# Performance work log

Hardware: AMD Instinct MI355X
Metric: run time of the kernel (lower is better)

Reference implementation:

```python
import jax, jax.numpy as jnp
import numpy as np

C = 64
N_H = 4
N_WIN = 16
WIN_L = 8   # compressor window length (overlapped)
WIN_S = 4   # compressor stride -> T//4 blocks


def _rms(x, eps=1e-6):
    return x * jax.lax.rsqrt(jnp.mean(x * x, axis=-1, keepdims=True) + eps)


def _rope(x, negate=False):
    # x: (..., L, D); rotate-half RoPE over positions 0..L-1
    L, D = x.shape[-2], x.shape[-1]
    half = D // 2
    inv_freq = 1.0 / (10000.0 ** (jnp.arange(half, dtype=x.dtype) / half))
    ang = jnp.arange(L, dtype=x.dtype)[:, None] * inv_freq  # (L, half)
    if negate:
        ang = -ang
    cos, sin = jnp.cos(ang), jnp.sin(ang)
    x1, x2 = x[..., :half], x[..., half:]
    return jnp.concatenate([x1 * cos - x2 * sin, x1 * sin + x2 * cos], axis=-1)


def _compress(H, W):
    # overlapped token compressor: windows of WIN_L, stride WIN_S, zero-pad tail
    B, T, d = H.shape
    Tc = T // WIN_S
    Hp = jnp.pad(H, ((0, 0), (0, WIN_L - WIN_S), (0, 0)))
    idx = WIN_S * jnp.arange(Tc)[:, None] + jnp.arange(WIN_L)[None, :]  # (Tc, WIN_L)
    win = Hp[:, idx]                       # (B, Tc, WIN_L, d)
    return win.reshape(B, Tc, WIN_L * d) @ W  # (B, Tc, out)


def setup_inputs() -> dict:
    key = jax.random.key(0)
    ks = jax.random.split(key, 11)
    B, T, d = 2, 2048, 256

    def w(k, shape, fan):
        return jax.random.normal(k, shape, jnp.float32) / np.float32(np.sqrt(fan))

    H = jax.random.normal(ks[0], (B, T, d), jnp.float32)
    return {
        'H': H,
        'Wc_comp': w(ks[1], (WIN_L * d, C), WIN_L * d),
        'Wc_idx': w(ks[2], (WIN_L * d, 32), WIN_L * d),
        'W_DQ': w(ks[3], (d, 64), d),
        'W_IUQ': w(ks[4], (64, 4 * 32), 64),
        'W_w': w(ks[5], (64, 4), 64),
        'W_Q': w(ks[6], (d, N_H * C), d),
        'W_KV': w(ks[7], (d, C), d),
        'g_q': jnp.ones((N_H, C), jnp.float32),
        'g_k': jnp.ones((C,), jnp.float32),
        'g_v': jnp.ones((C,), jnp.float32),
        'Wg0': w(ks[8], (2 * C, 64), 2 * C),
        'bg0': jnp.zeros((64,), jnp.float32),
        'Wg1': w(ks[9], (2 * C, 64), 2 * C),
        'bg1': jnp.zeros((64,), jnp.float32),
        'Wout': w(ks[10], (128, d), 128),
        'bout': jnp.zeros((d,), jnp.float32),
    }


def reference(H, Wc_comp, Wc_idx, W_DQ, W_IUQ, W_w, W_Q, W_KV,
              g_q, g_k, g_v, Wg0, bg0, Wg1, bg1, Wout, bout):
    B, T, d = H.shape
    Tc = T // 4
    k_top = min(8, Tc)

    # ---- lightning indexer ----
    H_dc = H @ W_DQ                                   # (B,T,64)
    Q_I = (H_dc @ W_IUQ).reshape(B, T, 4, 32)         # (B,T,4,32)
    W_Iw = (H_dc @ W_w)[..., None]                    # (B,T,4,1)
    K_I = _compress(H, Wc_idx)                        # (B,Tc,32)
    dot = jnp.einsum('bthc,bsc->bths', Q_I, K_I)      # (B,T,4,Tc)
    I_ts = (W_Iw * jax.nn.relu(dot)).sum(axis=2)      # (B,T,Tc)

    t = jnp.arange(T)[:, None]
    s = jnp.arange(Tc)[None, :]
    mask_I = jnp.where(4 * s <= t, 0.0, -jnp.inf)     # (T,Tc) causal over blocks
    _, topk_idx = jax.lax.top_k(I_ts + mask_I, k_top)  # (B,T,k)
    bI = jnp.arange(B)[:, None, None]
    tI = jnp.arange(T)[None, :, None]
    M_comp = jnp.full((B, T, Tc), -jnp.inf).at[bI, tI, topk_idx].set(0.0)

    # ---- compressed + sliding KV ----
    KV = jnp.concatenate([_compress(H, Wc_comp), H @ W_KV], axis=1)  # (B,Tc+T,C)

    Q = (H @ W_Q).reshape(B, T, N_H, C).transpose(0, 2, 1, 3)        # (B,nh,T,C)
    Q = _rms(Q) * g_q[None, :, None, :]
    K = _rms(KV) * g_k
    V = _rms(KV) * g_v
    Q = _rope(Q)
    K = _rope(K)
    V = _rope(V)

    S = jnp.einsum('bhtc,bsc->bhts', Q, K) / np.float32(np.sqrt(C))  # (B,nh,T,Tc+T)

    S_comp = S[..., :Tc] + M_comp[:, None]
    rel = t - jnp.arange(T)[None, :]
    mask_slide = jnp.where((rel >= 0) & (rel < N_WIN), 0.0, -jnp.inf)  # (T,T)
    S_slide = S[..., Tc:] + mask_slide

    P = jax.nn.softmax(jnp.concatenate([S_comp, S_slide], axis=-1), axis=-1)
    O = jnp.einsum('bhts,bsc->bhtc', P, V)            # (B,nh,T,C)
    O = _rope(O, negate=True)

    O0 = O[:, :2].transpose(0, 2, 1, 3).reshape(B, T, 2 * C)
    O1 = O[:, 2:].transpose(0, 2, 1, 3).reshape(B, T, 2 * C)
    p_all = jnp.concatenate([O0 @ Wg0 + bg0, O1 @ Wg1 + bg1], axis=-1)
    return p_all @ Wout + bout
```

## Files before the change

kernel.cpp:

```cpp
#include <hip/hip_runtime.h>
#include <hip/hip_bf16.h>
#include <math.h>

#define T_DIM 2048
#define B_DIM 2
#define D_DIM 256
#define TC 512
#define KV_LEN 2560

typedef __attribute__((ext_vector_type(8))) short bf16x8;
typedef __attribute__((ext_vector_type(4))) float f32x4;
typedef unsigned short ush;

__device__ __forceinline__ float wave_sum64(float v) {
#pragma unroll
    for (int off = 32; off > 0; off >>= 1) v += __shfl_xor(v, off, 64);
    return v;
}

__device__ __forceinline__ float rope_angle(int pos, int j) {
    float inv = powf(10000.0f, -(float)j * (1.0f / 32.0f));
    return (float)pos * inv;
}

__global__ __launch_bounds__(256) void k_prep(
    const float* __restrict__ H, const float* __restrict__ W_Q,
    const float* __restrict__ W_KV, const float* __restrict__ W_DQ,
    const float* __restrict__ Wc_comp, const float* __restrict__ Wc_idx,
    const float* __restrict__ Wg0, const float* __restrict__ bg0,
    const float* __restrict__ Wg1, const float* __restrict__ bg1,
    const float* __restrict__ Wout, const float* __restrict__ bout,
    ush* __restrict__ Ap, ush* __restrict__ Ac,
    ush* __restrict__ Bp, ush* __restrict__ Bc,
    ush* __restrict__ Bo, float* __restrict__ biascomb)
{
    int gid = blockIdx.x * 256 + threadIdx.x;
    float vals[8];
    ush* dst;
    bool lo_part;

    if (gid < 262144) {
        int tile = gid >> 10;
        int c = (gid >> 6) & 15;
        int l = gid & 63;
        int bt = tile * 16 + (l & 15);
        int kb = (c & 7) * 32 + (l >> 4) * 8;
        const float* src = H + (size_t)bt * 256 + kb;
#pragma unroll
        for (int j = 0; j < 8; ++j) vals[j] = src[j];
        lo_part = (c >= 8);
        dst = Ap + (size_t)gid * 8;
    } else if (gid < 786432) {
        int g = gid - 262144;
        int tile = g >> 13;
        int c = (g >> 6) & 127;
        int l = g & 63;
        int m = tile * 16 + (l & 15);
        int s = m & 511;
        int b = m >> 9;
        int k2b = (c & 63) * 32 + (l >> 4) * 8;
        int r4 = 4 * s + (k2b >> 8);
        int col = k2b & 255;
        if (r4 < T_DIM) {
            const float* src = H + ((size_t)b * T_DIM + r4) * 256 + col;
#pragma unroll
            for (int j = 0; j < 8; ++j) vals[j] = src[j];
        } else {
#pragma unroll
            for (int j = 0; j < 8; ++j) vals[j] = 0.f;
        }
        lo_part = (c >= 64);
        dst = Ac + (size_t)g * 8;
    } else if (gid < 811008) {
        int g = gid - 786432;
        int tile = g >> 10;
        int c = (g >> 6) & 15;
        int l = g & 63;
        int n = tile * 16 + (l & 15);
        int kb = (c & 7) * 32 + (l >> 4) * 8;
#pragma unroll
        for (int j = 0; j < 8; ++j) {
            int k = kb + j;
            float w;
            if (n < 256)      w = W_Q[(size_t)k * 256 + n];
            else if (n < 320) w = W_KV[(size_t)k * 64 + (n - 256)];
            else              w = W_DQ[(size_t)k * 64 + (n - 320)];
            vals[j] = w;
        }
        lo_part = (c >= 8);
        dst = Bp + (size_t)g * 8;
    } else if (gid < 860160) {
        int g = gid - 811008;
        int tile = g >> 13;
        int c = (g >> 6) & 127;
        int l = g & 63;
        int n = tile * 16 + (l & 15);
        int k2b = (c & 63) * 32 + (l >> 4) * 8;
#pragma unroll
        for (int j = 0; j < 8; ++j) {
            int k = k2b + j;
            vals[j] = (n < 64) ? Wc_comp[(size_t)k * 64 + n]
                               : Wc_idx[(size_t)k * 32 + (n - 64)];
        }
        lo_part = (c >= 64);
        dst = Bc + (size_t)g * 8;
    } else if (gid < 925696) {
        int g = gid - 860160;
        int k = g >> 8;
        int n = g & 255;
        float acc = 0.f;
        if (k < 128) {
            for (int i = 0; i < 64; ++i)
                acc = fmaf(Wg0[k * 64 + i], Wout[(size_t)i * 256 + n], acc);
        } else {
            for (int i = 0; i < 64; ++i)
                acc = fmaf(Wg1[(k - 128) * 64 + i], Wout[(size_t)(64 + i) * 256 + n], acc);
        }
        __hip_bfloat16 hb = __float2bfloat16(acc);
        float hif = __bfloat162float(hb);
        __hip_bfloat16 lb = __float2bfloat16(acc - hif);
        int tile = n >> 4;
        int chi = k >> 5;
        int lane2 = (n & 15) + 16 * ((k >> 3) & 3);
        int j = k & 7;
        Bo[(size_t)(tile * 16 + chi) * 512 + lane2 * 8 + j] = *(ush*)&hb;
        Bo[(size_t)(tile * 16 + chi + 8) * 512 + lane2 * 8 + j] = *(ush*)&lb;
        return;
    } else if (gid < 925952) {
        int n = gid - 925696;
        float acc = bout[n];
        for (int i = 0; i < 64; ++i) {
            acc = fmaf(bg0[i], Wout[(size_t)i * 256 + n], acc);
            acc = fmaf(bg1[i], Wout[(size_t)(64 + i) * 256 + n], acc);
        }
        biascomb[n] = acc;
        return;
    } else {
        return;
    }

    bf16x8 out8;
#pragma unroll
    for (int j = 0; j < 8; ++j) {
        float x = vals[j];
        __hip_bfloat16 hb = __float2bfloat16(x);
        if (!lo_part) {
            out8[j] = *(short*)&hb;
        } else {
            float hif = __bfloat162float(hb);
            __hip_bfloat16 lb = __float2bfloat16(x - hif);
            out8[j] = *(short*)&lb;
        }
    }
    *(bf16x8*)dst = out8;
}

__global__ __launch_bounds__(64) void k_mfma(
    const ush* __restrict__ Ap, const ush* __restrict__ Ac,
    const ush* __restrict__ Bp, const ush* __restrict__ Bc,
    float* __restrict__ Pre, float* __restrict__ Prec_part)
{
    int lane = threadIdx.x;
    int mrow = lane & 15;
    int q = lane >> 4;

    f32x4 acc[2][6];
#pragma unroll
    for (int mt = 0; mt < 2; ++mt)
#pragma unroll
        for (int nt = 0; nt < 6; ++nt) acc[mt][nt] = (f32x4){0.f, 0.f, 0.f, 0.f};

    if (blockIdx.x < 512) {
        int p = blockIdx.x;
        int m0 = (p >> 2) * 32;
        int n0 = (p & 3) * 96;
        int at0 = (m0 >> 4) * 16;
        int bt0n = (n0 >> 4) * 16;

        for (int c = 0; c < 8; ++c) {
            bf16x8 ahi[2], alo[2], bhi[6], blo[6];
#pragma unroll
            for (int mt = 0; mt < 2; ++mt) {
                ahi[mt] = *(const bf16x8*)(Ap + (size_t)((at0 + mt * 16) + c) * 512 + lane * 8);
                alo[mt] = *(const bf16x8*)(Ap + (size_t)((at0 + mt * 16) + 8 + c) * 512 + lane * 8);
            }
#pragma unroll
            for (int nt = 0; nt < 6; ++nt) {
                bhi[nt] = *(const bf16x8*)(Bp + (size_t)((bt0n + nt * 16) + c) * 512 + lane * 8);
                blo[nt] = *(const bf16x8*)(Bp + (size_t)((bt0n + nt * 16) + 8 + c) * 512 + lane * 8);
            }
#pragma unroll
            for (int mt = 0; mt < 2; ++mt)
#pragma unroll
                for (int nt = 0; nt < 6; ++nt) {
                    acc[mt][nt] = __builtin_amdgcn_mfma_f32_16x16x32_bf16(ahi[mt], bhi[nt], acc[mt][nt], 0, 0, 0);
                    acc[mt][nt] = __builtin_amdgcn_mfma_f32_16x16x32_bf16(ahi[mt], blo[nt], acc[mt][nt], 0, 0, 0);
                    acc[mt][nt] = __builtin_amdgcn_mfma_f32_16x16x32_bf16(alo[mt], bhi[nt], acc[mt][nt], 0, 0, 0);
                }
        }

#pragma unroll
        for (int mt = 0; mt < 2; ++mt)
#pragma unroll
            for (int nt = 0; nt < 6; ++nt)
#pragma unroll
                for (int reg = 0; reg < 4; ++reg)
                    Pre[(size_t)(m0 + 16 * mt + 4 * q + reg) * 384 + n0 + 16 * nt + mrow] =
                        acc[mt][nt][reg];
    } else {
        int cb = blockIdx.x - 512;
        int m0 = (cb >> 2) * 32;
        int q4 = cb & 3;
        int at0 = (m0 >> 4) * 128;

        for (int cl = 0; cl < 16; ++cl) {
            int c = q4 * 16 + cl;
            bf16x8 ahi[2], alo[2], bhi[6], blo[6];
#pragma unroll
            for (int mt = 0; mt < 2; ++mt) {
                ahi[mt] = *(const bf16x8*)(Ac + (size_t)((at0 + mt * 128) + c) * 512 + lane * 8);
                alo[mt] = *(const bf16x8*)(Ac + (size_t)((at0 + mt * 128) + 64 + c) * 512 + lane * 8);
            }
#pragma unroll
            for (int nt = 0; nt < 6; ++nt) {
                bhi[nt] = *(const bf16x8*)(Bc + (size_t)(nt * 128 + c) * 512 + lane * 8);
                blo[nt] = *(const bf16x8*)(Bc + (size_t)(nt * 128 + 64 + c) * 512 + lane * 8);
            }
#pragma unroll
            for (int mt = 0; mt < 2; ++mt)
#pragma unroll
                for (int nt = 0; nt < 6; ++nt) {
                    acc[mt][nt] = __builtin_amdgcn_mfma_f32_16x16x32_bf16(ahi[mt], bhi[nt], acc[mt][nt], 0, 0, 0);
                    acc[mt][nt] = __builtin_amdgcn_mfma_f32_16x16x32_bf16(ahi[mt], blo[nt], acc[mt][nt], 0, 0, 0);
                    acc[mt][nt] = __builtin_amdgcn_mfma_f32_16x16x32_bf16(alo[mt], bhi[nt], acc[mt][nt], 0, 0, 0);
                }
        }

        float* dst = Prec_part + (size_t)q4 * (1024 * 96);
#pragma unroll
        for (int mt = 0; mt < 2; ++mt)
#pragma unroll
            for (int nt = 0; nt < 6; ++nt)
#pragma unroll
                for (int reg = 0; reg < 4; ++reg)
                    dst[(size_t)(m0 + 16 * mt + 4 * q + reg) * 96 + 16 * nt + mrow] =
                        acc[mt][nt][reg];
    }
}

__global__ __launch_bounds__(256) void k_epi(
    const float* __restrict__ Pre, const float* __restrict__ Prec_part,
    const float* __restrict__ W_IUQ, const float* __restrict__ W_w,
    const float* __restrict__ g_q, const float* __restrict__ g_k,
    const float* __restrict__ g_v,
    float* __restrict__ QI, float* __restrict__ Wiw, float* __restrict__ Qr,
    float* __restrict__ KIbuf, float* __restrict__ Kbuf, float* __restrict__ Vbuf)
{
    __shared__ float sWI[8192];
    __shared__ float sWw[256];
    __shared__ float sHdc[4][64];

    int tid = threadIdx.x;
    int wv = tid >> 6;
    int lane = tid & 63;

    if (blockIdx.x < 1024) {
        int bt = blockIdx.x * 4 + wv;
        int b = bt >> 11;
        int t = bt & 2047;

        for (int i = tid * 4; i < 8192; i += 1024)
            *(float4*)&sWI[i] = *(const float4*)(W_IUQ + i);
        if (tid < 64) ((float4*)sWw)[tid] = ((const float4*)W_w)[tid];

        const float* pr = Pre + (size_t)bt * 384;
        sHdc[wv][lane] = pr[320 + lane];
        __syncthreads();

        int j = lane & 31;
        float s_t, c_t;
        sincosf(rope_angle(t, j), &s_t, &c_t);

#pragma unroll
        for (int r = 0; r < 4; ++r) {
            float qv = pr[r * 64 + lane];
            float ss = wave_sum64(qv * qv);
            float sc = rsqrtf(ss * (1.0f / 64.0f) + 1e-6f);
            float qq = qv * sc * g_q[r * 64 + lane];
            float prt = __shfl_xor(qq, 32, 64);
            float o = (lane < 32) ? fmaf(qq, c_t, -prt * s_t)
                                  : fmaf(prt, s_t, qq * c_t);
            Qr[(size_t)bt * 256 + r * 64 + lane] = o;
        }
        {
            float kvv = pr[256 + lane];
            float ss = wave_sum64(kvv * kvv);
            float sc = rsqrtf(ss * (1.0f / 64.0f) + 1e-6f);
            float kk = kvv * sc * g_k[lane];
            float vv = kvv * sc * g_v[lane];
            int pos = TC + t;
            float s_p, c_p;
            sincosf(rope_angle(pos, j), &s_p, &c_p);
            float pk = __shfl_xor(kk, 32, 64);
            float pv = __shfl_xor(vv, 32, 64);
            float ko = (lane < 32) ? fmaf(kk, c_p, -pk * s_p) : fmaf(pk, s_p, kk * c_p);
            float vo = (lane < 32) ? fmaf(vv, c_p, -pv * s_p) : fmaf(pv, s_p, vv * c_p);
            size_t off = ((size_t)b * KV_LEN + pos) * 64 + lane;
            Kbuf[off] = ko;
            Vbuf[off] = vo;
        }
        {
            float a0 = 0.f, a1 = 0.f;
#pragma unroll 8
            for (int jj = 0; jj < 64; ++jj) {
                float hv = sHdc[wv][jj];
                a0 = fmaf(hv, sWI[jj * 128 + lane], a0);
                a1 = fmaf(hv, sWI[jj * 128 + 64 + lane], a1);
            }
            QI[(size_t)bt * 128 + lane] = a0;
            QI[(size_t)bt * 128 + 64 + lane] = a1;
            if (lane < 4) {
                float aw = 0.f;
                for (int jj = 0; jj < 64; ++jj)
                    aw = fmaf(sHdc[wv][jj], sWw[jj * 4 + lane], aw);
                Wiw[(size_t)bt * 4 + lane] = aw;
            }
        }
    } else {
        int sg = (blockIdx.x - 1024) * 4 + wv;
        int b = sg >> 9;
        int s = sg & 511;

        const float* p0 = Prec_part + (size_t)sg * 96;
        float kvv = p0[lane] + p0[98304 + lane] + p0[2 * 98304 + lane] + p0[3 * 98304 + lane];

        float ss = wave_sum64(kvv * kvv);
        float sc = rsqrtf(ss * (1.0f / 64.0f) + 1e-6f);
        float kk = kvv * sc * g_k[lane];
        float vv = kvv * sc * g_v[lane];
        int j = lane & 31;
        float sa, ca;
        sincosf(rope_angle(s, j), &sa, &ca);
        float pk = __shfl_xor(kk, 32, 64);
        float pv = __shfl_xor(vv, 32, 64);
        float ko = (lane < 32) ? fmaf(kk, ca, -pk * sa) : fmaf(pk, sa, kk * ca);
        float vo = (lane < 32) ? fmaf(vv, ca, -pv * sa) : fmaf(pv, sa, vv * ca);
        size_t off = ((size_t)b * KV_LEN + s) * 64 + lane;
        Kbuf[off] = ko;
        Vbuf[off] = vo;

        if (lane < 32) {
            float a = p0[64 + lane] + p0[98304 + 64 + lane] +
                      p0[2 * 98304 + 64 + lane] + p0[3 * 98304 + 64 + lane];
            KIbuf[((size_t)b * TC + s) * 32 + lane] = a;
        }
    }
}

__global__ __launch_bounds__(256) void k_score_topk(
    const float* __restrict__ QI, const float* __restrict__ Wiw,
    const float* __restrict__ KIbuf, int* __restrict__ topk)
{
    int tid = threadIdx.x;
    int wv = tid >> 6;
    int lane = tid & 63;
    int bt0 = blockIdx.x * 4;
    int bt = bt0 + wv;
    int b = bt >> 11;
    int t = bt & 2047;

    __shared__ float sQ[4][128];
    __shared__ float sw[4][4];
    __shared__ float sKI[64 * 33];

    sQ[wv][lane] = QI[(size_t)bt * 128 + lane];
    sQ[wv][64 + lane] = QI[(size_t)bt * 128 + 64 + lane];
    if (lane < 4) sw[wv][lane] = Wiw[(size_t)bt * 4 + lane];

    const float* KIb = KIbuf + (size_t)b * TC * 32;
    int smax = t >> 2;
    int smax_blk = ((bt0 + 3) & 2047) >> 2;

    float vals[8];
#pragma unroll
    for (int r = 0; r < 8; ++r) vals[r] = -INFINITY;

    for (int r = 0; r < 8; ++r) {
        if (r * 64 > smax_blk) break;
        __syncthreads();
        for (int i = tid; i < 512; i += 256) {
            int row = i >> 3;
            int cseg = (i & 7) * 4;
            float4 v = *(const float4*)(KIb + (size_t)(r * 64 + row) * 32 + cseg);
            float* dst = &sKI[row * 33 + cseg];
            dst[0] = v.x; dst[1] = v.y; dst[2] = v.z; dst[3] = v.w;
        }
        __syncthreads();

        int s = r * 64 + lane;
        if (s <= smax) {
            float dd0 = 0.f, dd1 = 0.f, dd2 = 0.f, dd3 = 0.f;
#pragma unroll
            for (int c = 0; c < 32; ++c) {
                float kv = sKI[lane * 33 + c];
                dd0 = fmaf(sQ[wv][c], kv, dd0);
                dd1 = fmaf(sQ[wv][32 + c], kv, dd1);
                dd2 = fmaf(sQ[wv][64 + c], kv, dd2);
                dd3 = fmaf(sQ[wv][96 + c], kv, dd3);
            }
            vals[r] = sw[wv][0] * fmaxf(dd0, 0.f) + sw[wv][1] * fmaxf(dd1, 0.f) +
                      sw[wv][2] * fmaxf(dd2, 0.f) + sw[wv][3] * fmaxf(dd3, 0.f);
        }
    }

    unsigned consumed = 0u;
    for (int k2 = 0; k2 < 8; ++k2) {
        float bv = -INFINITY;
        int bi = 0x7fffffff;
#pragma unroll
        for (int r = 0; r < 8; ++r) {
            if (!(consumed & (1u << r))) {
                int s = lane + 64 * r;
                float v = vals[r];
                if (v > bv || (v == bv && s < bi)) { bv = v; bi = s; }
            }
        }
#pragma unroll
        for (int off = 1; off < 64; off <<= 1) {
            float ov = __shfl_xor(bv, off, 64);
            int oi = __shfl_xor(bi, off, 64);
            if (ov > bv || (ov == bv && oi < bi)) { bv = ov; bi = oi; }
        }
        if ((bi & 63) == lane) consumed |= 1u << (bi >> 6);
        if (lane == 0) topk[(size_t)bt * 8 + k2] = bi;
    }
}

__global__ __launch_bounds__(1024) void k_attn(
    const float* __restrict__ Qr, const float* __restrict__ Kbuf,
    const float* __restrict__ Vbuf, const int* __restrict__ topk,
    float* __restrict__ Obuf)
{
    int tid = threadIdx.x;
    int lt = tid >> 8;
    int t256 = tid & 255;
    int h = t256 >> 6;
    int lane = tid & 63;
    int bt = blockIdx.x * 4 + lt;
    int b = bt >> 11;
    int t = bt & 2047;

    __shared__ float sKV[4][48 * 65];
    __shared__ float sQ[4][256];
    __shared__ int sPos[4][24];
    __shared__ float sP[4][4][24];

    sQ[lt][t256] = Qr[(size_t)bt * 256 + t256];
    if (t256 < 8) {
        sPos[lt][t256] = topk[(size_t)bt * 8 + t256];
    } else if (t256 < 24) {
        int rel = t256 - 8;
        int sp = t - rel;
        sPos[lt][t256] = (sp >= 0) ? (TC + sp) : -1;
    }
    __syncthreads();

    for (int i = t256; i < 768; i += 256) {
        int row = i >> 4;
        int seg = (i & 15) << 2;
        int key = (row < 24) ? row : row - 24;
        int pos = sPos[lt][key];
        if (pos >= 0) {
            const float* src = ((row < 24) ? Kbuf : Vbuf) +
                               ((size_t)b * KV_LEN + pos) * 64 + seg;
            float4 v = *(const float4*)src;
            float* dst = &sKV[lt][row * 65 + seg];
            dst[0] = v.x; dst[1] = v.y; dst[2] = v.z; dst[3] = v.w;
        }
    }
    __syncthreads();

    float scv = -INFINITY;
    if (lane < 24) {
        int pos = sPos[lt][lane];
        if (pos >= 0) {
            float dd = 0.f;
#pragma unroll
            for (int c = 0; c < 64; ++c)
                dd = fmaf(sQ[lt][h * 64 + c], sKV[lt][lane * 65 + c], dd);
            scv = dd * 0.125f;
        }
    }
    float m = scv;
#pragma unroll
    for (int off = 1; off < 64; off <<= 1) m = fmaxf(m, __shfl_xor(m, off, 64));
    float p = expf(scv - m);
    if (scv == -INFINITY) p = 0.f;
    float l = p;
#pragma unroll
    for (int off = 1; off < 64; off <<= 1) l += __shfl_xor(l, off, 64);
    p /= l;
    if (lane < 24) sP[lt][h][lane] = p;

    float o = 0.f;
#pragma unroll
    for (int j2 = 0; j2 < 24; ++j2) {
        int pos = sPos[lt][j2];
        if (pos >= 0)
            o = fmaf(sP[lt][h][j2], sKV[lt][(24 + j2) * 65 + lane], o);
    }

    int j = lane & 31;
    float sa, ca;
    sincosf(rope_angle(t, j), &sa, &ca);
    float prt = __shfl_xor(o, 32, 64);
    float oo = (lane < 32) ? fmaf(o, ca, prt * sa) : fmaf(-prt, sa, o * ca);
    Obuf[(size_t)bt * 256 + h * 64 + lane] = oo;
}

__global__ __launch_bounds__(256) void k_cvtO(
    const float* __restrict__ Obuf, ush* __restrict__ Ao)
{
    int gid = blockIdx.x * 256 + threadIdx.x;
    int tile = gid >> 10;
    int c = (gid >> 6) & 15;
    int l = gid & 63;
    int row = tile * 16 + (l & 15);
    int kb = (c & 7) * 32 + (l >> 4) * 8;
    const float* src = Obuf + (size_t)row * 256 + kb;
    bool lo_part = (c >= 8);
    bf16x8 out8;
#pragma unroll
    for (int j = 0; j < 8; ++j) {
        float x = src[j];
        __hip_bfloat16 hb = __float2bfloat16(x);
        if (!lo_part) {
            out8[j] = *(short*)&hb;
        } else {
            float hif = __bfloat162float(hb);
            __hip_bfloat16 lb = __float2bfloat16(x - hif);
            out8[j] = *(short*)&lb;
        }
    }
    *(bf16x8*)(Ao + (size_t)gid * 8) = out8;
}

__global__ __launch_bounds__(64) void k_out(
    const ush* __restrict__ Ao, const ush* __restrict__ Bo,
    const float* __restrict__ biascomb, float* __restrict__ out)
{
    int lane = threadIdx.x;
    int mrow = lane & 15;
    int q = lane >> 4;
    int p = blockIdx.x;
    int m0 = (p >> 2) * 32;
    int n0 = (p & 3) * 64;
    int at0 = (m0 >> 4) * 16;
    int bt0n = (n0 >> 4) * 16;

    f32x4 acc[2][4];
#pragma unroll
    for (int mt = 0; mt < 2; ++mt)
#pragma unroll
        for (int nt = 0; nt < 4; ++nt) acc[mt][nt] = (f32x4){0.f, 0.f, 0.f, 0.f};

    for (int c = 0; c < 8; ++c) {
        bf16x8 ahi[2], alo[2], bhi[4], blo[4];
#pragma unroll
        for (int mt = 0; mt < 2; ++mt) {
            ahi[mt] = *(const bf16x8*)(Ao + (size_t)((at0 + mt * 16) + c) * 512 + lane * 8);
            alo[mt] = *(const bf16x8*)(Ao + (size_t)((at0 + mt * 16) + 8 + c) * 512 + lane * 8);
        }
#pragma unroll
        for (int nt = 0; nt < 4; ++nt) {
            bhi[nt] = *(const bf16x8*)(Bo + (size_t)((bt0n + nt * 16) + c) * 512 + lane * 8);
            blo[nt] = *(const bf16x8*)(Bo + (size_t)((bt0n + nt * 16) + 8 + c) * 512 + lane * 8);
        }
#pragma unroll
        for (int mt = 0; mt < 2; ++mt)
#pragma unroll
            for (int nt = 0; nt < 4; ++nt) {
                acc[mt][nt] = __builtin_amdgcn_mfma_f32_16x16x32_bf16(ahi[mt], bhi[nt], acc[mt][nt], 0, 0, 0);
                acc[mt][nt] = __builtin_amdgcn_mfma_f32_16x16x32_bf16(ahi[mt], blo[nt], acc[mt][nt], 0, 0, 0);
                acc[mt][nt] = __builtin_amdgcn_mfma_f32_16x16x32_bf16(alo[mt], bhi[nt], acc[mt][nt], 0, 0, 0);
            }
    }

#pragma unroll
    for (int mt = 0; mt < 2; ++mt)
#pragma unroll
        for (int nt = 0; nt < 4; ++nt) {
            float bia = biascomb[n0 + 16 * nt + mrow];
#pragma unroll
            for (int reg = 0; reg < 4; ++reg)
                out[(size_t)(m0 + 16 * mt + 4 * q + reg) * 256 + n0 + 16 * nt + mrow] =
                    acc[mt][nt][reg] + bia;
        }
}

extern "C" void kernel_launch(void* const* d_in, const int* in_sizes, int n_in,
                              void* d_out, int out_size, void* d_ws, size_t ws_size,
                              hipStream_t stream) {
    const float* H       = (const float*)d_in[0];
    const float* Wc_comp = (const float*)d_in[1];
    const float* Wc_idx  = (const float*)d_in[2];
    const float* W_DQ    = (const float*)d_in[3];
    const float* W_IUQ   = (const float*)d_in[4];
    const float* W_w     = (const float*)d_in[5];
    const float* W_Q     = (const float*)d_in[6];
    const float* W_KV    = (const float*)d_in[7];
    const float* g_q     = (const float*)d_in[8];
    const float* g_k     = (const float*)d_in[9];
    const float* g_v     = (const float*)d_in[10];
    const float* Wg0     = (const float*)d_in[11];
    const float* bg0     = (const float*)d_in[12];
    const float* Wg1     = (const float*)d_in[13];
    const float* bg1     = (const float*)d_in[14];
    const float* Wout    = (const float*)d_in[15];
    const float* bout    = (const float*)d_in[16];

    float* ws  = (float*)d_ws;
    float* QI    = ws;
    float* Qr    = ws + 524288;
    float* Wiw   = ws + 1572864;
    float* KI    = ws + 1589248;
    float* Kb    = ws + 1622016;
    float* Vb    = ws + 1949696;
    int*   topkb = (int*)(ws + 2277376);
    float* Pre   = ws + 2310144;
    float* Prec  = ws + 3883008;
    ush* Ap = (ush*)(ws + 4276224);
    ush* Ac = (ush*)(ws + 5324800);
    ush* Bp = (ush*)(ws + 7421952);
    ush* Bc = (ush*)(ws + 7520256);
    ush* Bo = (ush*)(ws + 7716864);
    float* biascomb = ws + 7782400;
    float* Obuf = ws + 4276224;
    ush*   Ao   = (ush*)(ws + 5324800);

    float* outp = (float*)d_out;

    hipLaunchKernelGGL(k_prep, dim3(3617), dim3(256), 0, stream,
                       H, W_Q, W_KV, W_DQ, Wc_comp, Wc_idx,
                       Wg0, bg0, Wg1, bg1, Wout, bout,
                       Ap, Ac, Bp, Bc, Bo, biascomb);
    hipLaunchKernelGGL(k_mfma, dim3(640), dim3(64), 0, stream,
                       Ap, Ac, Bp, Bc, Pre, Prec);
    hipLaunchKernelGGL(k_epi, dim3(1280), dim3(256), 0, stream,
                       Pre, Prec, W_IUQ, W_w, g_q, g_k, g_v,
                       QI, Wiw, Qr, KI, Kb, Vb);
    hipLaunchKernelGGL(k_score_topk, dim3((B_DIM * T_DIM) / 4), dim3(256), 0, stream,
                       QI, Wiw, KI, topkb);
    hipLaunchKernelGGL(k_attn, dim3((B_DIM * T_DIM) / 4), dim3(1024), 0, stream,
                       Qr, Kb, Vb, topkb, Obuf);
    hipLaunchKernelGGL(k_cvtO, dim3(1024), dim3(256), 0, stream,
                       Obuf, Ao);
    hipLaunchKernelGGL(k_out, dim3(512), dim3(64), 0, stream,
                       Ao, Bo, biascomb, outp);
}
```

Measured before the change: 182.5 us.

## Fold index-query projection into GEMM, fuse topk with attention, fuse O conversion

```diff
diff --git a/kernel.cpp b/kernel.cpp
--- a/kernel.cpp
+++ b/kernel.cpp
@@ -26,6 +26,7 @@
 __global__ __launch_bounds__(256) void k_prep(
     const float* __restrict__ H, const float* __restrict__ W_Q,
     const float* __restrict__ W_KV, const float* __restrict__ W_DQ,
+    const float* __restrict__ W_IUQ, const float* __restrict__ W_w,
     const float* __restrict__ Wc_comp, const float* __restrict__ Wc_idx,
     const float* __restrict__ Wg0, const float* __restrict__ bg0,
     const float* __restrict__ Wg1, const float* __restrict__ bg1,
@@ -71,7 +72,7 @@
         }
         lo_part = (c >= 64);
         dst = Ac + (size_t)g * 8;
-    } else if (gid < 811008) {
+    } else if (gid < 819200) {
         int g = gid - 786432;
         int tile = g >> 10;
         int c = (g >> 6) & 15;
@@ -84,13 +85,23 @@
             float w;
             if (n < 256)      w = W_Q[(size_t)k * 256 + n];
             else if (n < 320) w = W_KV[(size_t)k * 64 + (n - 256)];
-            else              w = W_DQ[(size_t)k * 64 + (n - 320)];
+            else if (n < 448) {
+                w = 0.f;
+                for (int i = 0; i < 64; ++i)
+                    w = fmaf(W_DQ[(size_t)k * 64 + i], W_IUQ[(size_t)i * 128 + (n - 320)], w);
+            } else if (n < 452) {
+                w = 0.f;
+                for (int i = 0; i < 64; ++i)
+                    w = fmaf(W_DQ[(size_t)k * 64 + i], W_w[(size_t)i * 4 + (n - 448)], w);
+            } else {
+                w = 0.f;
+            }
             vals[j] = w;
         }
         lo_part = (c >= 8);
         dst = Bp + (size_t)g * 8;
-    } else if (gid < 860160) {
-        int g = gid - 811008;
+    } else if (gid < 868352) {
+        int g = gid - 819200;
         int tile = g >> 13;
         int c = (g >> 6) & 127;
         int l = g & 63;
@@ -104,8 +115,8 @@
         }
         lo_part = (c >= 64);
         dst = Bc + (size_t)g * 8;
-    } else if (gid < 925696) {
-        int g = gid - 860160;
+    } else if (gid < 933888) {
+        int g = gid - 868352;
         int k = g >> 8;
         int n = g & 255;
         float acc = 0.f;
@@ -126,8 +137,8 @@
         Bo[(size_t)(tile * 16 + chi) * 512 + lane2 * 8 + j] = *(ush*)&hb;
         Bo[(size_t)(tile * 16 + chi + 8) * 512 + lane2 * 8 + j] = *(ush*)&lb;
         return;
-    } else if (gid < 925952) {
-        int n = gid - 925696;
+    } else if (gid < 934144) {
+        int n = gid - 933888;
         float acc = bout[n];
         for (int i = 0; i < 64; ++i) {
             acc = fmaf(bg0[i], Wout[(size_t)i * 256 + n], acc);
@@ -164,35 +175,35 @@
     int mrow = lane & 15;
     int q = lane >> 4;
 
-    f32x4 acc[2][6];
-#pragma unroll
-    for (int mt = 0; mt < 2; ++mt)
-#pragma unroll
-        for (int nt = 0; nt < 6; ++nt) acc[mt][nt] = (f32x4){0.f, 0.f, 0.f, 0.f};
-
     if (blockIdx.x < 512) {
         int p = blockIdx.x;
         int m0 = (p >> 2) * 32;
-        int n0 = (p & 3) * 96;
+        int n0 = (p & 3) * 128;
         int at0 = (m0 >> 4) * 16;
         int bt0n = (n0 >> 4) * 16;
 
+        f32x4 acc[2][8];
+#pragma unroll
+        for (int mt = 0; mt < 2; ++mt)
+#pragma unroll
+            for (int nt = 0; nt < 8; ++nt) acc[mt][nt] = (f32x4){0.f, 0.f, 0.f, 0.f};
+
         for (int c = 0; c < 8; ++c) {
-            bf16x8 ahi[2], alo[2], bhi[6], blo[6];
+            bf16x8 ahi[2], alo[2], bhi[8], blo[8];
 #pragma unroll
             for (int mt = 0; mt < 2; ++mt) {
                 ahi[mt] = *(const bf16x8*)(Ap + (size_t)((at0 + mt * 16) + c) * 512 + lane * 8);
                 alo[mt] = *(const bf16x8*)(Ap + (size_t)((at0 + mt * 16) + 8 + c) * 512 + lane * 8);
             }
 #pragma unroll
-            for (int nt = 0; nt < 6; ++nt) {
+            for (int nt = 0; nt < 8; ++nt) {
                 bhi[nt] = *(const bf16x8*)(Bp + (size_t)((bt0n + nt * 16) + c) * 512 + lane * 8);
                 blo[nt] = *(const bf16x8*)(Bp + (size_t)((bt0n + nt * 16) + 8 + c) * 512 + lane * 8);
             }
 #pragma unroll
             for (int mt = 0; mt < 2; ++mt)
 #pragma unroll
-                for (int nt = 0; nt < 6; ++nt) {
+                for (int nt = 0; nt < 8; ++nt) {
                     acc[mt][nt] = __builtin_amdgcn_mfma_f32_16x16x32_bf16(ahi[mt], bhi[nt], acc[mt][nt], 0, 0, 0);
                     acc[mt][nt] = __builtin_amdgcn_mfma_f32_16x16x32_bf16(ahi[mt], blo[nt], acc[mt][nt], 0, 0, 0);
                     acc[mt][nt] = __builtin_amdgcn_mfma_f32_16x16x32_bf16(alo[mt], bhi[nt], acc[mt][nt], 0, 0, 0);
@@ -202,10 +213,10 @@
 #pragma unroll
         for (int mt = 0; mt < 2; ++mt)
 #pragma unroll
-            for (int nt = 0; nt < 6; ++nt)
+            for (int nt = 0; nt < 8; ++nt)
 #pragma unroll
                 for (int reg = 0; reg < 4; ++reg)
-                    Pre[(size_t)(m0 + 16 * mt + 4 * q + reg) * 384 + n0 + 16 * nt + mrow] =
+                    Pre[(size_t)(m0 + 16 * mt + 4 * q + reg) * 512 + n0 + 16 * nt + mrow] =
                         acc[mt][nt][reg];
     } else {
         int cb = blockIdx.x - 512;
@@ -213,6 +224,12 @@
         int q4 = cb & 3;
         int at0 = (m0 >> 4) * 128;
 
+        f32x4 acc[2][6];
+#pragma unroll
+        for (int mt = 0; mt < 2; ++mt)
+#pragma unroll
+            for (int nt = 0; nt < 6; ++nt) acc[mt][nt] = (f32x4){0.f, 0.f, 0.f, 0.f};
+
         for (int cl = 0; cl < 16; ++cl) {
             int c = q4 * 16 + cl;
             bf16x8 ahi[2], alo[2], bhi[6], blo[6];
@@ -250,16 +267,11 @@
 
 __global__ __launch_bounds__(256) void k_epi(
     const float* __restrict__ Pre, const float* __restrict__ Prec_part,
-    const float* __restrict__ W_IUQ, const float* __restrict__ W_w,
     const float* __restrict__ g_q, const float* __restrict__ g_k,
     const float* __restrict__ g_v,
-    float* __restrict__ QI, float* __restrict__ Wiw, float* __restrict__ Qr,
-    float* __restrict__ KIbuf, float* __restrict__ Kbuf, float* __restrict__ Vbuf)
+    float* __restrict__ Qr, float* __restrict__ KIbuf,
+    float* __restrict__ Kbuf, float* __restrict__ Vbuf)
 {
-    __shared__ float sWI[8192];
-    __shared__ float sWw[256];
-    __shared__ float sHdc[4][64];
-
     int tid = threadIdx.x;
     int wv = tid >> 6;
     int lane = tid & 63;
@@ -269,14 +281,7 @@
         int b = bt >> 11;
         int t = bt & 2047;
 
-        for (int i = tid * 4; i < 8192; i += 1024)
-            *(float4*)&sWI[i] = *(const float4*)(W_IUQ + i);
-        if (tid < 64) ((float4*)sWw)[tid] = ((const float4*)W_w)[tid];
-
-        const float* pr = Pre + (size_t)bt * 384;
-        sHdc[wv][lane] = pr[320 + lane];
-        __syncthreads();
-
+        const float* pr = Pre + (size_t)bt * 512;
         int j = lane & 31;
         float s_t, c_t;
         sincosf(rope_angle(t, j), &s_t, &c_t);
@@ -309,23 +314,6 @@
             Kbuf[off] = ko;
             Vbuf[off] = vo;
         }
-        {
-            float a0 = 0.f, a1 = 0.f;
-#pragma unroll 8
-            for (int jj = 0; jj < 64; ++jj) {
-                float hv = sHdc[wv][jj];
-                a0 = fmaf(hv, sWI[jj * 128 + lane], a0);
-                a1 = fmaf(hv, sWI[jj * 128 + 64 + lane], a1);
-            }
-            QI[(size_t)bt * 128 + lane] = a0;
-            QI[(size_t)bt * 128 + 64 + lane] = a1;
-            if (lane < 4) {
-                float aw = 0.f;
-                for (int jj = 0; jj < 64; ++jj)
-                    aw = fmaf(sHdc[wv][jj], sWw[jj * 4 + lane], aw);
-                Wiw[(size_t)bt * 4 + lane] = aw;
-            }
-        }
     } else {
         int sg = (blockIdx.x - 1024) * 4 + wv;
         int b = sg >> 9;
@@ -357,9 +345,10 @@
     }
 }
 
-__global__ __launch_bounds__(256) void k_score_topk(
-    const float* __restrict__ QI, const float* __restrict__ Wiw,
-    const float* __restrict__ KIbuf, int* __restrict__ topk)
+__global__ __launch_bounds__(256) void k_sparse(
+    const float* __restrict__ Pre, const float* __restrict__ KIbuf,
+    const float* __restrict__ Qr, const float* __restrict__ Kbuf,
+    const float* __restrict__ Vbuf, float* __restrict__ Obuf)
 {
     int tid = threadIdx.x;
     int wv = tid >> 6;
@@ -369,13 +358,17 @@
     int b = bt >> 11;
     int t = bt & 2047;
 
-    __shared__ float sQ[4][128];
-    __shared__ float sw[4][4];
-    __shared__ float sKI[64 * 33];
-
-    sQ[wv][lane] = QI[(size_t)bt * 128 + lane];
-    sQ[wv][64 + lane] = QI[(size_t)bt * 128 + 64 + lane];
-    if (lane < 4) sw[wv][lane] = Wiw[(size_t)bt * 4 + lane];
+    __shared__ float sBig[12480];
+    __shared__ float sQI[4][128];
+    __shared__ float swv[4][4];
+    __shared__ float sQr[4][256];
+    __shared__ float sP[4][4][24];
+    __shared__ int sPos[4][24];
+
+    const float* pr = Pre + (size_t)bt * 512;
+    sQI[wv][lane] = pr[320 + lane];
+    sQI[wv][64 + lane] = pr[384 + lane];
+    if (lane < 4) swv[wv][lane] = pr[448 + lane];
 
     const float* KIb = KIbuf + (size_t)b * TC * 32;
     int smax = t >> 2;
@@ -392,8 +385,8 @@
             int row = i >> 3;
             int cseg = (i & 7) * 4;
             float4 v = *(const float4*)(KIb + (size_t)(r * 64 + row) * 32 + cseg);
-            float* dst = &sKI[row * 33 + cseg];
-            dst[0] = v.x; dst[1] = v.y; dst[2] = v.z; dst[3] = v.w;
+            float* dstp = &sBig[row * 33 + cseg];
+            dstp[0] = v.x; dstp[1] = v.y; dstp[2] = v.z; dstp[3] = v.w;
         }
         __syncthreads();
 
@@ -402,14 +395,14 @@
             float dd0 = 0.f, dd1 = 0.f, dd2 = 0.f, dd3 = 0.f;
 #pragma unroll
             for (int c = 0; c < 32; ++c) {
-                float kv = sKI[lane * 33 + c];
-                dd0 = fmaf(sQ[wv][c], kv, dd0);
-                dd1 = fmaf(sQ[wv][32 + c], kv, dd1);
-                dd2 = fmaf(sQ[wv][64 + c], kv, dd2);
-                dd3 = fmaf(sQ[wv][96 + c], kv, dd3);
-            }
-            vals[r] = sw[wv][0] * fmaxf(dd0, 0.f) + sw[wv][1] * fmaxf(dd1, 0.f) +
-                      sw[wv][2] * fmaxf(dd2, 0.f) + sw[wv][3] * fmaxf(dd3, 0.f);
+                float kv = sBig[lane * 33 + c];
+                dd0 = fmaf(sQI[wv][c], kv, dd0);
+                dd1 = fmaf(sQI[wv][32 + c], kv, dd1);
+                dd2 = fmaf(sQI[wv][64 + c], kv, dd2);
+                dd3 = fmaf(sQI[wv][96 + c], kv, dd3);
+            }
+            vals[r] = swv[wv][0] * fmaxf(dd0, 0.f) + swv[wv][1] * fmaxf(dd1, 0.f) +
+                      swv[wv][2] * fmaxf(dd2, 0.f) + swv[wv][3] * fmaxf(dd3, 0.f);
         }
     }
 
@@ -432,121 +425,80 @@
             if (ov > bv || (ov == bv && oi < bi)) { bv = ov; bi = oi; }
         }
         if ((bi & 63) == lane) consumed |= 1u << (bi >> 6);
-        if (lane == 0) topk[(size_t)bt * 8 + k2] = bi;
-    }
-}
-
-__global__ __launch_bounds__(1024) void k_attn(
-    const float* __restrict__ Qr, const float* __restrict__ Kbuf,
-    const float* __restrict__ Vbuf, const int* __restrict__ topk,
-    float* __restrict__ Obuf)
-{
-    int tid = threadIdx.x;
-    int lt = tid >> 8;
-    int t256 = tid & 255;
-    int h = t256 >> 6;
-    int lane = tid & 63;
-    int bt = blockIdx.x * 4 + lt;
-    int b = bt >> 11;
-    int t = bt & 2047;
-
-    __shared__ float sKV[4][48 * 65];
-    __shared__ float sQ[4][256];
-    __shared__ int sPos[4][24];
-    __shared__ float sP[4][4][24];
-
-    sQ[lt][t256] = Qr[(size_t)bt * 256 + t256];
-    if (t256 < 8) {
-        sPos[lt][t256] = topk[(size_t)bt * 8 + t256];
-    } else if (t256 < 24) {
-        int rel = t256 - 8;
+        if (lane == 0) sPos[wv][k2] = bi;
+    }
+    if (lane >= 8 && lane < 24) {
+        int rel = lane - 8;
         int sp = t - rel;
-        sPos[lt][t256] = (sp >= 0) ? (TC + sp) : -1;
+        sPos[wv][lane] = (sp >= 0) ? (TC + sp) : -1;
     }
     __syncthreads();
 
-    for (int i = t256; i < 768; i += 256) {
-        int row = i >> 4;
-        int seg = (i & 15) << 2;
-        int key = (row < 24) ? row : row - 24;
-        int pos = sPos[lt][key];
-        if (pos >= 0) {
-            const float* src = ((row < 24) ? Kbuf : Vbuf) +
-                               ((size_t)b * KV_LEN + pos) * 64 + seg;
-            float4 v = *(const float4*)src;
-            float* dst = &sKV[lt][row * 65 + seg];
-            dst[0] = v.x; dst[1] = v.y; dst[2] = v.z; dst[3] = v.w;
-        }
-    }
+    float (*sKV)[48 * 65] = (float (*)[48 * 65])sBig;
+#pragma unroll
+    for (int lt = 0; lt < 4; ++lt) {
+        for (int i = tid; i < 768; i += 256) {
+            int row = i >> 4;
+            int seg = (i & 15) << 2;
+            int key = (row < 24) ? row : row - 24;
+            int pos = sPos[lt][key];
+            if (pos >= 0) {
+                const float* src = ((row < 24) ? Kbuf : Vbuf) +
+                                   ((size_t)b * KV_LEN + pos) * 64 + seg;
+                float4 v = *(const float4*)src;
+                float* dstp = &sKV[lt][row * 65 + seg];
+                dstp[0] = v.x; dstp[1] = v.y; dstp[2] = v.z; dstp[3] = v.w;
+            }
+        }
+    }
+    for (int i = tid; i < 1024; i += 256)
+        sQr[i >> 8][i & 255] = Qr[(size_t)(bt0 + (i >> 8)) * 256 + (i & 255)];
     __syncthreads();
-
-    float scv = -INFINITY;
-    if (lane < 24) {
-        int pos = sPos[lt][lane];
-        if (pos >= 0) {
-            float dd = 0.f;
-#pragma unroll
-            for (int c = 0; c < 64; ++c)
-                dd = fmaf(sQ[lt][h * 64 + c], sKV[lt][lane * 65 + c], dd);
-            scv = dd * 0.125f;
-        }
-    }
-    float m = scv;
-#pragma unroll
-    for (int off = 1; off < 64; off <<= 1) m = fmaxf(m, __shfl_xor(m, off, 64));
-    float p = expf(scv - m);
-    if (scv == -INFINITY) p = 0.f;
-    float l = p;
-#pragma unroll
-    for (int off = 1; off < 64; off <<= 1) l += __shfl_xor(l, off, 64);
-    p /= l;
-    if (lane < 24) sP[lt][h][lane] = p;
-
-    float o = 0.f;
-#pragma unroll
-    for (int j2 = 0; j2 < 24; ++j2) {
-        int pos = sPos[lt][j2];
-        if (pos >= 0)
-            o = fmaf(sP[lt][h][j2], sKV[lt][(24 + j2) * 65 + lane], o);
-    }
 
     int j = lane & 31;
     float sa, ca;
     sincosf(rope_angle(t, j), &sa, &ca);
-    float prt = __shfl_xor(o, 32, 64);
-    float oo = (lane < 32) ? fmaf(o, ca, prt * sa) : fmaf(-prt, sa, o * ca);
-    Obuf[(size_t)bt * 256 + h * 64 + lane] = oo;
-}
-
-__global__ __launch_bounds__(256) void k_cvtO(
-    const float* __restrict__ Obuf, ush* __restrict__ Ao)
-{
-    int gid = blockIdx.x * 256 + threadIdx.x;
-    int tile = gid >> 10;
-    int c = (gid >> 6) & 15;
-    int l = gid & 63;
-    int row = tile * 16 + (l & 15);
-    int kb = (c & 7) * 32 + (l >> 4) * 8;
-    const float* src = Obuf + (size_t)row * 256 + kb;
-    bool lo_part = (c >= 8);
-    bf16x8 out8;
-#pragma unroll
-    for (int j = 0; j < 8; ++j) {
-        float x = src[j];
-        __hip_bfloat16 hb = __float2bfloat16(x);
-        if (!lo_part) {
-            out8[j] = *(short*)&hb;
-        } else {
-            float hif = __bfloat162float(hb);
-            __hip_bfloat16 lb = __float2bfloat16(x - hif);
-            out8[j] = *(short*)&lb;
-        }
-    }
-    *(bf16x8*)(Ao + (size_t)gid * 8) = out8;
+
+#pragma unroll
+    for (int h = 0; h < 4; ++h) {
+        float scv = -INFINITY;
+        if (lane < 24) {
+            int pos = sPos[wv][lane];
+            if (pos >= 0) {
+                float dd = 0.f;
+#pragma unroll
+                for (int c = 0; c < 64; ++c)
+                    dd = fmaf(sQr[wv][h * 64 + c], sKV[wv][lane * 65 + c], dd);
+                scv = dd * 0.125f;
+            }
+        }
+        float m = scv;
+#pragma unroll
+        for (int off = 1; off < 64; off <<= 1) m = fmaxf(m, __shfl_xor(m, off, 64));
+        float p = expf(scv - m);
+        if (scv == -INFINITY) p = 0.f;
+        float l = p;
+#pragma unroll
+        for (int off = 1; off < 64; off <<= 1) l += __shfl_xor(l, off, 64);
+        p /= l;
+        if (lane < 24) sP[wv][h][lane] = p;
+
+        float o = 0.f;
+#pragma unroll
+        for (int j2 = 0; j2 < 24; ++j2) {
+            int pos = sPos[wv][j2];
+            if (pos >= 0)
+                o = fmaf(sP[wv][h][j2], sKV[wv][(24 + j2) * 65 + lane], o);
+        }
+
+        float prt = __shfl_xor(o, 32, 64);
+        float oo = (lane < 32) ? fmaf(o, ca, prt * sa) : fmaf(-prt, sa, o * ca);
+        Obuf[(size_t)bt * 256 + h * 64 + lane] = oo;
+    }
 }
 
 __global__ __launch_bounds__(64) void k_out(
-    const ush* __restrict__ Ao, const ush* __restrict__ Bo,
+    const float* __restrict__ Obuf, const ush* __restrict__ Bo,
     const float* __restrict__ biascomb, float* __restrict__ out)
 {
     int lane = threadIdx.x;
@@ -555,7 +507,6 @@
     int p = blockIdx.x;
     int m0 = (p >> 2) * 32;
     int n0 = (p & 3) * 64;
-    int at0 = (m0 >> 4) * 16;
     int bt0n = (n0 >> 4) * 16;
 
     f32x4 acc[2][4];
@@ -568,8 +519,18 @@
         bf16x8 ahi[2], alo[2], bhi[4], blo[4];
 #pragma unroll
         for (int mt = 0; mt < 2; ++mt) {
-            ahi[mt] = *(const bf16x8*)(Ao + (size_t)((at0 + mt * 16) + c) * 512 + lane * 8);
-            alo[mt] = *(const bf16x8*)(Ao + (size_t)((at0 + mt * 16) + 8 + c) * 512 + lane * 8);
+            const float* src = Obuf + (size_t)(m0 + 16 * mt + mrow) * 256 + c * 32 + 8 * q;
+            float4 x0 = *(const float4*)src;
+            float4 x1 = *(const float4*)(src + 4);
+            float xs[8] = {x0.x, x0.y, x0.z, x0.w, x1.x, x1.y, x1.z, x1.w};
+#pragma unroll
+            for (int j = 0; j < 8; ++j) {
+                __hip_bfloat16 hb = __float2bfloat16(xs[j]);
+                float hif = __bfloat162float(hb);
+                __hip_bfloat16 lb = __float2bfloat16(xs[j] - hif);
+                ahi[mt][j] = *(short*)&hb;
+                alo[mt][j] = *(short*)&lb;
+            }
         }
 #pragma unroll
         for (int nt = 0; nt < 4; ++nt) {
@@ -619,42 +580,33 @@
     const float* Wout    = (const float*)d_in[15];
     const float* bout    = (const float*)d_in[16];
 
-    float* ws  = (float*)d_ws;
-    float* QI    = ws;
-    float* Qr    = ws + 524288;
-    float* Wiw   = ws + 1572864;
-    float* KI    = ws + 1589248;
-    float* Kb    = ws + 1622016;
-    float* Vb    = ws + 1949696;
-    int*   topkb = (int*)(ws + 2277376);
-    float* Pre   = ws + 2310144;
-    float* Prec  = ws + 3883008;
-    ush* Ap = (ush*)(ws + 4276224);
-    ush* Ac = (ush*)(ws + 5324800);
-    ush* Bp = (ush*)(ws + 7421952);
-    ush* Bc = (ush*)(ws + 7520256);
-    ush* Bo = (ush*)(ws + 7716864);
-    float* biascomb = ws + 7782400;
-    float* Obuf = ws + 4276224;
-    ush*   Ao   = (ush*)(ws + 5324800);
+    float* ws = (float*)d_ws;
+    float* Qr   = ws;
+    float* KI   = ws + 1048576;
+    float* Kb   = ws + 1081344;
+    float* Vb   = ws + 1409024;
+    float* Pre  = ws + 1736704;
+    float* Prec = ws + 3833856;
+    float* Obuf = ws + 4227072;
+    ush* Ap = (ush*)(ws + 5275648);
+    ush* Ac = (ush*)(ws + 6324224);
+    ush* Bp = (ush*)(ws + 8421376);
+    ush* Bc = (ush*)(ws + 8552448);
+    ush* Bo = (ush*)(ws + 8749056);
+    float* biascomb = ws + 8814592;
 
     float* outp = (float*)d_out;
 
-    hipLaunchKernelGGL(k_prep, dim3(3617), dim3(256), 0, stream,
-                       H, W_Q, W_KV, W_DQ, Wc_comp, Wc_idx,
+    hipLaunchKernelGGL(k_prep, dim3(3649), dim3(256), 0, stream,
+                       H, W_Q, W_KV, W_DQ, W_IUQ, W_w, Wc_comp, Wc_idx,
                        Wg0, bg0, Wg1, bg1, Wout, bout,
                        Ap, Ac, Bp, Bc, Bo, biascomb);
     hipLaunchKernelGGL(k_mfma, dim3(640), dim3(64), 0, stream,
                        Ap, Ac, Bp, Bc, Pre, Prec);
     hipLaunchKernelGGL(k_epi, dim3(1280), dim3(256), 0, stream,
-                       Pre, Prec, W_IUQ, W_w, g_q, g_k, g_v,
-                       QI, Wiw, Qr, KI, Kb, Vb);
-    hipLaunchKernelGGL(k_score_topk, dim3((B_DIM * T_DIM) / 4), dim3(256), 0, stream,
-                       QI, Wiw, KI, topkb);
-    hipLaunchKernelGGL(k_attn, dim3((B_DIM * T_DIM) / 4), dim3(1024), 0, stream,
-                       Qr, Kb, Vb, topkb, Obuf);
-    hipLaunchKernelGGL(k_cvtO, dim3(1024), dim3(256), 0, stream,
-                       Obuf, Ao);
+                       Pre, Prec, g_q, g_k, g_v, Qr, KI, Kb, Vb);
+    hipLaunchKernelGGL(k_sparse, dim3(1024), dim3(256), 0, stream,
+                       Pre, KI, Qr, Kb, Vb, Obuf);
     hipLaunchKernelGGL(k_out, dim3(512), dim3(64), 0, stream,
-                       Ao, Bo, biascomb, outp);
-}
+                       Obuf, Bo, biascomb, outp);
+}
```

New measurement: 204.5 us. 12.1% more time.
